# Kernel tuning notes

Hardware: AMD Instinct MI355X
Metric: run time of the kernel (lower is better)

## Reference

```python
import jax, jax.numpy as jnp
import numpy as np

B, D, H = 16384, 1024, 16
HD = D // H
EPS = 1e-5


def setup_inputs() -> dict:
    key = jax.random.key(0)
    ks = jax.random.split(key, 16)
    w = lambda k, shape: jax.random.normal(k, shape, jnp.float32) * 0.02
    return {
        "img_emb": jax.random.normal(ks[0], (B, D), jnp.float32),
        "txt_emb": jax.random.normal(ks[1], (B, D), jnp.float32),
        "route_choice": jax.random.randint(ks[2], (B,), 0, 3, jnp.int32),
        # gate: Linear(2D -> D) + sigmoid
        "Wg": w(ks[3], (2 * D, D)), "bg": jnp.zeros((D,), jnp.float32),
        # MultiheadAttention in/out projections
        "Wqkv": w(ks[4], (D, 3 * D)), "bqkv": jnp.zeros((3 * D,), jnp.float32),
        "Wo": w(ks[5], (D, D)), "bo": jnp.zeros((D,), jnp.float32),
        # LayerNorm
        "gamma": jnp.ones((D,), jnp.float32), "beta": jnp.zeros((D,), jnp.float32),
        # FFN: Linear(D->4D), GELU, Linear(4D->D)
        "Wf1": w(ks[6], (D, 4 * D)), "bf1": jnp.zeros((4 * D,), jnp.float32),
        "Wf2": w(ks[7], (4 * D, D)), "bf2": jnp.zeros((D,), jnp.float32),
    }


def _layernorm(x, gamma, beta):
    mu = jnp.mean(x, axis=-1, keepdims=True)
    var = jnp.mean(jnp.square(x - mu), axis=-1, keepdims=True)
    return (x - mu) * jax.lax.rsqrt(var + EPS) * gamma + beta


def reference(img_emb, txt_emb, route_choice, Wg, bg, Wqkv, bqkv, Wo, bo,
              gamma, beta, Wf1, bf1, Wf2, bf2):
    # Eval mode: energy_loss = 0, no dropout. Routing choice supplied as int input.
    # Compute the 'full' fusion branch densely, then select per sample.
    ri = jnp.concatenate([img_emb, txt_emb], axis=-1)          # [B, 2D]
    gate = jax.nn.sigmoid(ri @ Wg + bg)                        # [B, D]
    fused = gate * img_emb + (1.0 - gate) * txt_emb            # [B, D]

    x = jnp.stack([img_emb, txt_emb], axis=1)                  # [B, 2, D]
    qkv = x @ Wqkv + bqkv                                      # [B, 2, 3D]
    q, k, v = jnp.split(qkv, 3, axis=-1)
    q = q.reshape(B, 2, H, HD)
    k = k.reshape(B, 2, H, HD)
    v = v.reshape(B, 2, H, HD)
    scores = jnp.einsum("bqhd,bkhd->bhqk", q, k) / np.sqrt(HD) # [B, H, 2, 2]
    attn = jax.nn.softmax(scores, axis=-1)
    ctx = jnp.einsum("bhqk,bkhd->bqhd", attn, v).reshape(B, 2, D)
    attn_out = ctx @ Wo + bo                                   # [B, 2, D]

    fused = fused + attn_out.mean(axis=1)
    fused = _layernorm(fused, gamma, beta)
    full_out = jax.nn.gelu(fused @ Wf1 + bf1, approximate=False) @ Wf2 + bf2

    rc = route_choice[:, None]
    out = jnp.where(rc == 0, img_emb, jnp.where(rc == 1, txt_emb, full_out))
    return out
```

## Files before the change

kernel.cpp:

```cpp
#include <hip/hip_runtime.h>
#include <hip/hip_bf16.h>
#include <math.h>

#define NB 16384
#define DIM 1024
#define CAP 6656
#define MT 52

using bf16 = __hip_bfloat16;
typedef __attribute__((ext_vector_type(8))) short short8;
typedef __attribute__((ext_vector_type(4))) short short4v;
typedef __attribute__((ext_vector_type(4))) float float4v;

__device__ __forceinline__ void gl_lds16(const void* g, void* l) {
  __builtin_amdgcn_global_load_lds(
      (const __attribute__((address_space(1))) unsigned int*)g,
      (__attribute__((address_space(3))) unsigned int*)l, 16, 0, 0);
}

__device__ __forceinline__ short f2bf(float x) {
  __hip_bfloat16 h = __float2bfloat16(x);
  return *reinterpret_cast<short*>(&h);
}

__device__ __forceinline__ void swz(int bid, int nN, int& m0, int& n0) {
  int x = bid & 7;
  int r = bid >> 3;
  int nl = nN >> 3;
  int nLoc = r % nl;
  int m = r / nl;
  n0 = (x + 8 * nLoc) * 128;
  m0 = m * 128;
}

__global__ __launch_bounds__(256) void transpose_cast(
    const float* __restrict__ in, bf16* __restrict__ out, int K, int N) {
  __shared__ float tile[32][33];
  int n0 = blockIdx.x * 32, k0 = blockIdx.y * 32;
  int tx = threadIdx.x, ty = threadIdx.y;
#pragma unroll
  for (int i = 0; i < 32; i += 8)
    tile[ty + i][tx] = in[(size_t)(k0 + ty + i) * N + n0 + tx];
  __syncthreads();
#pragma unroll
  for (int i = 0; i < 32; i += 8)
    out[(size_t)(n0 + ty + i) * K + k0 + tx] = __float2bfloat16(tile[tx][ty + i]);
}

__global__ __launch_bounds__(256) void fill_bias(const float* __restrict__ bqkv,
                                                 const float* __restrict__ bg,
                                                 float* __restrict__ biasA,
                                                 float* __restrict__ biasB) {
  int i = blockIdx.x * 256 + threadIdx.x;
  float qv = (i < 3072) ? bqkv[i] : 0.f;
  biasA[i] = qv;
  biasB[i] = (i < 3072) ? qv : bg[i - 3072];
}

__global__ void zero_cnt(int* cnt) { if (threadIdx.x == 0) *cnt = 0; }

__global__ __launch_bounds__(256) void index_build(const int* __restrict__ route,
                                                   int* __restrict__ cnt,
                                                   int* __restrict__ idx,
                                                   int* __restrict__ pos) {
  int r = blockIdx.x * 256 + threadIdx.x;
  if (r < NB && route[r] == 2) {
    int p = atomicAdd(cnt, 1);
    idx[p] = r;
    pos[r] = p;
  }
}

__global__ __launch_bounds__(256) void gather_cast(
    const float* __restrict__ img, const float* __restrict__ txt,
    const int* __restrict__ cnt, const int* __restrict__ idx,
    bf16* __restrict__ xg, bf16* __restrict__ tg) {
  int n = blockIdx.x;
  if (n >= *cnt) return;
  int r = idx[n];
  int c = threadIdx.x * 4;
  float4 vi = *(const float4*)(img + (size_t)r * DIM + c);
  float4 vt = *(const float4*)(txt + (size_t)r * DIM + c);
  short4v pi, pt;
  pi[0] = f2bf(vi.x); pi[1] = f2bf(vi.y); pi[2] = f2bf(vi.z); pi[3] = f2bf(vi.w);
  pt[0] = f2bf(vt.x); pt[1] = f2bf(vt.y); pt[2] = f2bf(vt.z); pt[3] = f2bf(vt.w);
  *(short4v*)(xg + (size_t)n * DIM + c) = pi;
  *(short4v*)(tg + (size_t)n * DIM + c) = pt;
}

__global__ __launch_bounds__(256) void gemm_qkvg(
    const bf16* __restrict__ A0, const bf16* __restrict__ BtQ,
    const bf16* __restrict__ BtG, const float* __restrict__ bias,
    bf16* __restrict__ outp, const int* __restrict__ cntp) {
  const int cnt = *cntp;
  int m0, n0;
  swz(blockIdx.x, 32, m0, n0);
  if (m0 >= ((cnt + 127) & ~127)) return;
  alignas(16) __shared__ bf16 sA[128 * 32];
  alignas(16) __shared__ bf16 sB[128 * 32];
  const int t = threadIdx.x;
  const int wave = t >> 6, lane = t & 63;
  const int wm = (wave >> 1) * 64, wn = (wave & 1) * 64;
  const int r16 = lane & 15, quad = lane >> 4;
  const bf16* Bt = (n0 < 3072) ? BtQ + (size_t)n0 * 1024 : BtG + (size_t)(n0 - 3072) * 1024;

  float4v acc[4][4] = {};
  for (int k0 = 0; k0 < 1024; k0 += 32) {
    if (k0) __syncthreads();
#pragma unroll
    for (int j = 0; j < 2; ++j) {
      int c = t + j * 256;
      int row = c >> 2;
      int kk = k0 + (c & 3) * 8;
      gl_lds16(Bt + (size_t)row * 1024 + kk, (void*)(sB + j * 2048 + wave * 512));
      gl_lds16(A0 + (size_t)(m0 + row) * 1024 + kk, (void*)(sA + j * 2048 + wave * 512));
    }
    __syncthreads();
    short8 af[4], bfr[4];
#pragma unroll
    for (int i = 0; i < 4; ++i) {
      af[i] = *(const short8*)(sA + (wm + i * 16 + r16) * 32 + quad * 8);
      bfr[i] = *(const short8*)(sB + (wn + i * 16 + r16) * 32 + quad * 8);
    }
#pragma unroll
    for (int i = 0; i < 4; ++i)
#pragma unroll
      for (int j = 0; j < 4; ++j)
        acc[i][j] =
            __builtin_amdgcn_mfma_f32_16x16x32_bf16(af[i], bfr[j], acc[i][j], 0, 0, 0);
  }
#pragma unroll
  for (int i = 0; i < 4; ++i)
#pragma unroll
    for (int j = 0; j < 4; ++j) {
      int gcol = n0 + wn + j * 16 + r16;
      float bv = bias[gcol];
#pragma unroll
      for (int r = 0; r < 4; ++r) {
        int grow = m0 + wm + i * 16 + quad * 4 + r;
        outp[(size_t)grow * 4096 + gcol] = __float2bfloat16(acc[i][j][r] + bv);
      }
    }
}

__global__ __launch_bounds__(256) void attn_kernel(const bf16* __restrict__ qx,
                                                   const bf16* __restrict__ tx,
                                                   bf16* __restrict__ cmean,
                                                   const int* __restrict__ cntp) {
  const int cnt = *cntp;
  int gw = blockIdx.x * 4 + (threadIdx.x >> 6);
  int lane = threadIdx.x & 63;
  int n = gw >> 4, h = gw & 15;
  if (n >= ((cnt + 127) & ~127)) return;
  const bf16* b0 = qx + (size_t)n * 4096 + h * 64 + lane;
  const bf16* b1 = tx + (size_t)n * 4096 + h * 64 + lane;
  float q0 = __bfloat162float(b0[0]);
  float k0 = __bfloat162float(b0[1024]);
  float v0 = __bfloat162float(b0[2048]);
  float q1 = __bfloat162float(b1[0]);
  float k1 = __bfloat162float(b1[1024]);
  float v1 = __bfloat162float(b1[2048]);
  float s00 = q0 * k0, s01 = q0 * k1, s10 = q1 * k0, s11 = q1 * k1;
#pragma unroll
  for (int d = 32; d > 0; d >>= 1) {
    s00 += __shfl_xor(s00, d);
    s01 += __shfl_xor(s01, d);
    s10 += __shfl_xor(s10, d);
    s11 += __shfl_xor(s11, d);
  }
  const float sc = 0.125f;
  s00 *= sc; s01 *= sc; s10 *= sc; s11 *= sc;
  float m0 = fmaxf(s00, s01), m1 = fmaxf(s10, s11);
  float e00 = expf(s00 - m0), e01 = expf(s01 - m0);
  float e10 = expf(s10 - m1), e11 = expf(s11 - m1);
  float i0 = 1.f / (e00 + e01), i1 = 1.f / (e10 + e11);
  float c0 = (e00 * i0) * v0 + (e01 * i0) * v1;
  float c1 = (e10 * i1) * v0 + (e11 * i1) * v1;
  cmean[(size_t)n * DIM + h * 64 + lane] = __float2bfloat16(0.5f * (c0 + c1));
}

__global__ __launch_bounds__(256) void wo_z_kernel(
    const float* __restrict__ img, const float* __restrict__ txt,
    const bf16* __restrict__ qx, const bf16* __restrict__ tx,
    const bf16* __restrict__ WoT, const float* __restrict__ bg,
    const float* __restrict__ bo, const bf16* __restrict__ cmean,
    bf16* __restrict__ z, const int* __restrict__ cntp, const int* __restrict__ idx) {
  const int cnt = *cntp;
  int m0, n0;
  swz(blockIdx.x, 8, m0, n0);
  if (m0 >= ((cnt + 127) & ~127)) return;
  alignas(16) __shared__ bf16 sA[128 * 32];
  alignas(16) __shared__ bf16 sB[128 * 32];
  const int t = threadIdx.x;
  const int wave = t >> 6, lane = t & 63;
  const int wm = (wave >> 1) * 64, wn = (wave & 1) * 64;
  const int r16 = lane & 15, quad = lane >> 4;

  float4v acc[4][4] = {};
  for (int k0 = 0; k0 < 1024; k0 += 32) {
    if (k0) __syncthreads();
#pragma unroll
    for (int j = 0; j < 2; ++j) {
      int c = t + j * 256;
      int row = c >> 2;
      int kk = k0 + (c & 3) * 8;
      gl_lds16(WoT + (size_t)(n0 + row) * 1024 + kk, (void*)(sB + j * 2048 + wave * 512));
      gl_lds16(cmean + (size_t)(m0 + row) * 1024 + kk, (void*)(sA + j * 2048 + wave * 512));
    }
    __syncthreads();
    short8 af[4], bfr[4];
#pragma unroll
    for (int i = 0; i < 4; ++i) {
      af[i] = *(const short8*)(sA + (wm + i * 16 + r16) * 32 + quad * 8);
      bfr[i] = *(const short8*)(sB + (wn + i * 16 + r16) * 32 + quad * 8);
    }
#pragma unroll
    for (int i = 0; i < 4; ++i)
#pragma unroll
      for (int j = 0; j < 4; ++j)
        acc[i][j] =
            __builtin_amdgcn_mfma_f32_16x16x32_bf16(af[i], bfr[j], acc[i][j], 0, 0, 0);
  }
#pragma unroll
  for (int i = 0; i < 4; ++i)
#pragma unroll
    for (int j = 0; j < 4; ++j) {
      int gcol = n0 + wn + j * 16 + r16;
      float bgv = bg[gcol], bov = bo[gcol];
#pragma unroll
      for (int r = 0; r < 4; ++r) {
        int grow = m0 + wm + i * 16 + quad * 4 + r;
        float zv = 0.f;
        if (grow < cnt) {
          int orow = idx[grow];
          float gp = __bfloat162float(qx[(size_t)grow * 4096 + 3072 + gcol]) +
                     __bfloat162float(tx[(size_t)grow * 4096 + 3072 + gcol]) + bgv;
          float g = 1.f / (1.f + expf(-gp));
          size_t ii = (size_t)orow * DIM + gcol;
          float fm = g * img[ii] + (1.f - g) * txt[ii];
          zv = fm + acc[i][j][r] + bov;
        }
        z[(size_t)grow * DIM + gcol] = __float2bfloat16(zv);
      }
    }
}

__global__ __launch_bounds__(256) void ln_kernel(bf16* __restrict__ z,
                                                 const float* __restrict__ g,
                                                 const float* __restrict__ be,
                                                 const int* __restrict__ cntp) {
  const int cnt = *cntp;
  int b = blockIdx.x, t = threadIdx.x;
  if (b >= ((cnt + 127) & ~127)) return;
  bf16* zr = z + (size_t)b * DIM;
  float v[4];
  float s = 0.f, s2 = 0.f;
#pragma unroll
  for (int i = 0; i < 4; ++i) {
    float x = __bfloat162float(zr[t + 256 * i]);
    v[i] = x; s += x; s2 += x * x;
  }
#pragma unroll
  for (int d = 32; d > 0; d >>= 1) {
    s += __shfl_xor(s, d);
    s2 += __shfl_xor(s2, d);
  }
  __shared__ float rs[4], rs2[4];
  int w = t >> 6, lane = t & 63;
  if (!lane) { rs[w] = s; rs2[w] = s2; }
  __syncthreads();
  s = rs[0] + rs[1] + rs[2] + rs[3];
  s2 = rs2[0] + rs2[1] + rs2[2] + rs2[3];
  float mu = s * (1.f / 1024.f);
  float var = s2 * (1.f / 1024.f) - mu * mu;
  float r = rsqrtf(var + 1e-5f);
#pragma unroll
  for (int i = 0; i < 4; ++i) {
    int c = t + 256 * i;
    zr[c] = __float2bfloat16((v[i] - mu) * r * g[c] + be[c]);
  }
}

__global__ __launch_bounds__(256) void gemm_gelu(
    const bf16* __restrict__ A0, const bf16* __restrict__ Bt,
    const float* __restrict__ bias, bf16* __restrict__ outp,
    const int* __restrict__ cntp) {
  const int cnt = *cntp;
  int m0, n0;
  swz(blockIdx.x, 32, m0, n0);
  if (m0 >= ((cnt + 127) & ~127)) return;
  alignas(16) __shared__ bf16 sA[128 * 32];
  alignas(16) __shared__ bf16 sB[128 * 32];
  const int t = threadIdx.x;
  const int wave = t >> 6, lane = t & 63;
  const int wm = (wave >> 1) * 64, wn = (wave & 1) * 64;
  const int r16 = lane & 15, quad = lane >> 4;

  float4v acc[4][4] = {};
  for (int k0 = 0; k0 < 1024; k0 += 32) {
    if (k0) __syncthreads();
#pragma unroll
    for (int j = 0; j < 2; ++j) {
      int c = t + j * 256;
      int row = c >> 2;
      int kk = k0 + (c & 3) * 8;
      gl_lds16(Bt + (size_t)(n0 + row) * 1024 + kk, (void*)(sB + j * 2048 + wave * 512));
      gl_lds16(A0 + (size_t)(m0 + row) * 1024 + kk, (void*)(sA + j * 2048 + wave * 512));
    }
    __syncthreads();
    short8 af[4], bfr[4];
#pragma unroll
    for (int i = 0; i < 4; ++i) {
      af[i] = *(const short8*)(sA + (wm + i * 16 + r16) * 32 + quad * 8);
      bfr[i] = *(const short8*)(sB + (wn + i * 16 + r16) * 32 + quad * 8);
    }
#pragma unroll
    for (int i = 0; i < 4; ++i)
#pragma unroll
      for (int j = 0; j < 4; ++j)
        acc[i][j] =
            __builtin_amdgcn_mfma_f32_16x16x32_bf16(af[i], bfr[j], acc[i][j], 0, 0, 0);
  }
#pragma unroll
  for (int i = 0; i < 4; ++i)
#pragma unroll
    for (int j = 0; j < 4; ++j) {
      int gcol = n0 + wn + j * 16 + r16;
      float bv = bias[gcol];
#pragma unroll
      for (int r = 0; r < 4; ++r) {
        int grow = m0 + wm + i * 16 + quad * 4 + r;
        float v = acc[i][j][r] + bv;
        float gl = 0.5f * v * (1.f + erff(v * 0.70710678118654752f));
        outp[(size_t)grow * 4096 + gcol] = __float2bfloat16(gl);
      }
    }
}

__global__ __launch_bounds__(256) void gemm_splitk(
    const bf16* __restrict__ A0, const bf16* __restrict__ Bt,
    float* __restrict__ parts, const int* __restrict__ cntp) {
  const int cnt = *cntp;
  const int nblk = 8 * MT;
  int s = blockIdx.x / nblk;
  int bid = blockIdx.x % nblk;
  int m0, n0;
  swz(bid, 8, m0, n0);
  if (m0 >= ((cnt + 127) & ~127)) return;
  alignas(16) __shared__ bf16 sA[128 * 32];
  alignas(16) __shared__ bf16 sB[128 * 32];
  const int t = threadIdx.x;
  const int wave = t >> 6, lane = t & 63;
  const int wm = (wave >> 1) * 64, wn = (wave & 1) * 64;
  const int r16 = lane & 15, quad = lane >> 4;
  const int kbase = s * 2048;

  float4v acc[4][4] = {};
  for (int k0 = kbase; k0 < kbase + 2048; k0 += 32) {
    if (k0 != kbase) __syncthreads();
#pragma unroll
    for (int j = 0; j < 2; ++j) {
      int c = t + j * 256;
      int row = c >> 2;
      int kk = k0 + (c & 3) * 8;
      gl_lds16(Bt + (size_t)(n0 + row) * 4096 + kk, (void*)(sB + j * 2048 + wave * 512));
      gl_lds16(A0 + (size_t)(m0 + row) * 4096 + kk, (void*)(sA + j * 2048 + wave * 512));
    }
    __syncthreads();
    short8 af[4], bfr[4];
#pragma unroll
    for (int i = 0; i < 4; ++i) {
      af[i] = *(const short8*)(sA + (wm + i * 16 + r16) * 32 + quad * 8);
      bfr[i] = *(const short8*)(sB + (wn + i * 16 + r16) * 32 + quad * 8);
    }
#pragma unroll
    for (int i = 0; i < 4; ++i)
#pragma unroll
      for (int j = 0; j < 4; ++j)
        acc[i][j] =
            __builtin_amdgcn_mfma_f32_16x16x32_bf16(af[i], bfr[j], acc[i][j], 0, 0, 0);
  }
  float* out = parts + (size_t)s * CAP * 1024;
#pragma unroll
  for (int i = 0; i < 4; ++i)
#pragma unroll
    for (int j = 0; j < 4; ++j) {
      int gcol = n0 + wn + j * 16 + r16;
#pragma unroll
      for (int r = 0; r < 4; ++r) {
        int grow = m0 + wm + i * 16 + quad * 4 + r;
        out[(size_t)grow * 1024 + gcol] = acc[i][j][r];
      }
    }
}

__global__ __launch_bounds__(256) void route_out(
    const float* __restrict__ img, const float* __restrict__ txt,
    const int* __restrict__ route, const int* __restrict__ pos,
    const float* __restrict__ parts, const float* __restrict__ bf2,
    float* __restrict__ out) {
  int row = blockIdx.x;
  int rc = route[row];
  int c = threadIdx.x * 4;
  float4 v;
  if (rc == 2) {
    int n = pos[row];
    float4 p0 = *(const float4*)(parts + (size_t)n * 1024 + c);
    float4 p1 = *(const float4*)(parts + (size_t)CAP * 1024 + (size_t)n * 1024 + c);
    float4 b = *(const float4*)(bf2 + c);
    v.x = p0.x + p1.x + b.x;
    v.y = p0.y + p1.y + b.y;
    v.z = p0.z + p1.z + b.z;
    v.w = p0.w + p1.w + b.w;
  } else {
    const float* src = (rc == 0) ? img : txt;
    v = *(const float4*)(src + (size_t)row * DIM + c);
  }
  *(float4*)(out + (size_t)row * DIM + c) = v;
}

extern "C" void kernel_launch(void* const* d_in, const int* in_sizes, int n_in,
                              void* d_out, int out_size, void* d_ws, size_t ws_size,
                              hipStream_t stream) {
  const float* img = (const float*)d_in[0];
  const float* txt = (const float*)d_in[1];
  const int* route = (const int*)d_in[2];
  const float* Wg = (const float*)d_in[3];
  const float* bg = (const float*)d_in[4];
  const float* Wqkv = (const float*)d_in[5];
  const float* bqkv = (const float*)d_in[6];
  const float* Wo = (const float*)d_in[7];
  const float* bo = (const float*)d_in[8];
  const float* gamma = (const float*)d_in[9];
  const float* beta = (const float*)d_in[10];
  const float* Wf1 = (const float*)d_in[11];
  const float* bf1 = (const float*)d_in[12];
  const float* Wf2 = (const float*)d_in[13];
  const float* bf2 = (const float*)d_in[14];

  char* ws = (char*)d_ws;
  size_t off = 0;
  auto alloc = [&](size_t bytes) {
    char* p = ws + off;
    off += (bytes + 255) & ~(size_t)255;
    return p;
  };
  int* cntp = (int*)alloc(256);
  int* idx = (int*)alloc((size_t)NB * 4);
  int* pos = (int*)alloc((size_t)NB * 4);
  float* biasA = (float*)alloc(4096 * 4);
  float* biasB = (float*)alloc(4096 * 4);
  bf16* WqkvT = (bf16*)alloc((size_t)3072 * 1024 * 2);
  bf16* WgTopT = (bf16*)alloc((size_t)1024 * 1024 * 2);
  bf16* WgBotT = (bf16*)alloc((size_t)1024 * 1024 * 2);
  bf16* WoT = (bf16*)alloc((size_t)1024 * 1024 * 2);
  bf16* Wf1T = (bf16*)alloc((size_t)4096 * 1024 * 2);
  bf16* Wf2T = (bf16*)alloc((size_t)1024 * 4096 * 2);
  bf16* xg = (bf16*)alloc((size_t)CAP * 1024 * 2);
  bf16* tg = (bf16*)alloc((size_t)CAP * 1024 * 2);
  bf16* qx = (bf16*)alloc((size_t)CAP * 4096 * 2);
  bf16* tx = (bf16*)alloc((size_t)CAP * 4096 * 2);
  bf16* cmean = (bf16*)alloc((size_t)CAP * 1024 * 2);
  bf16* zb = (bf16*)alloc((size_t)CAP * 1024 * 2);
  bf16* hb = qx;
  float* parts = (float*)tx;

  dim3 tblk(32, 8);
  transpose_cast<<<dim3(3072 / 32, 1024 / 32), tblk, 0, stream>>>(Wqkv, WqkvT, 1024, 3072);
  transpose_cast<<<dim3(1024 / 32, 1024 / 32), tblk, 0, stream>>>(Wg, WgTopT, 1024, 1024);
  transpose_cast<<<dim3(1024 / 32, 1024 / 32), tblk, 0, stream>>>(Wg + 1024 * 1024, WgBotT, 1024, 1024);
  transpose_cast<<<dim3(1024 / 32, 1024 / 32), tblk, 0, stream>>>(Wo, WoT, 1024, 1024);
  transpose_cast<<<dim3(4096 / 32, 1024 / 32), tblk, 0, stream>>>(Wf1, Wf1T, 1024, 4096);
  transpose_cast<<<dim3(1024 / 32, 4096 / 32), tblk, 0, stream>>>(Wf2, Wf2T, 4096, 1024);
  fill_bias<<<16, 256, 0, stream>>>(bqkv, bg, biasA, biasB);

  zero_cnt<<<1, 64, 0, stream>>>(cntp);
  index_build<<<NB / 256, 256, 0, stream>>>(route, cntp, idx, pos);
  gather_cast<<<CAP, 256, 0, stream>>>(img, txt, cntp, idx, xg, tg);

  gemm_qkvg<<<32 * MT, 256, 0, stream>>>(xg, WqkvT, WgTopT, biasA, qx, cntp);
  gemm_qkvg<<<32 * MT, 256, 0, stream>>>(tg, WqkvT, WgBotT, biasB, tx, cntp);
  attn_kernel<<<CAP * 4, 256, 0, stream>>>(qx, tx, cmean, cntp);
  wo_z_kernel<<<8 * MT, 256, 0, stream>>>(img, txt, qx, tx, WoT, bg, bo, cmean, zb,
                                          cntp, idx);
  ln_kernel<<<CAP, 256, 0, stream>>>(zb, gamma, beta, cntp);
  gemm_gelu<<<32 * MT, 256, 0, stream>>>(zb, Wf1T, bf1, hb, cntp);
  gemm_splitk<<<2 * 8 * MT, 256, 0, stream>>>(hb, Wf2T, parts, cntp);
  route_out<<<NB, 256, 0, stream>>>(img, txt, route, pos, parts, bf2, (float*)d_out);
}
```

Baseline: 595.7 us.

## Fuse prep kernels, swizzle LDS tiles, merge QKV GEMMs, atomic split-K output

Merges the six weight transpose-casts, the bias fill and the counter reset into one prep kernel to cut launch count. Applies an XOR swizzle to the LDS tile layout in every GEMM, so fragment reads avoid bank conflicts. Merges the two QKV/gate GEMMs into a single 2D-grid launch. Replaces the split-K partial buffer and the route_out combine with a pre-fill of the output (passthrough rows or bias) plus atomicAdd scatter from the split-K GEMM, which adds atomic traffic and makes the summation order nondeterministic.

```diff
diff --git a/kernel.cpp b/kernel.cpp
--- a/kernel.cpp
+++ b/kernel.cpp
@@ -33,41 +33,64 @@
   m0 = m * 128;
 }
 
-__global__ __launch_bounds__(256) void transpose_cast(
-    const float* __restrict__ in, bf16* __restrict__ out, int K, int N) {
-  __shared__ float tile[32][33];
-  int n0 = blockIdx.x * 32, k0 = blockIdx.y * 32;
+#define STAGE_TILE(SRC, LD, DST)                                              \
+  {                                                                           \
+    int row = c >> 2, sslot = c & 3;                                          \
+    int kp = sslot ^ (row & 3);                                               \
+    gl_lds16((SRC) + (size_t)row * (LD) + k0 + kp * 8,                        \
+             (void*)((DST) + j * 2048 + wave * 512));                         \
+  }
+
+__device__ __forceinline__ void tr_tile(const float* in, bf16* out, int K, int N,
+                                        int tile) {
+  __shared__ float tl[32][33];
+  int nx = N / 32;
+  int n0 = (tile % nx) * 32, k0 = (tile / nx) * 32;
   int tx = threadIdx.x, ty = threadIdx.y;
 #pragma unroll
   for (int i = 0; i < 32; i += 8)
-    tile[ty + i][tx] = in[(size_t)(k0 + ty + i) * N + n0 + tx];
+    tl[ty + i][tx] = in[(size_t)(k0 + ty + i) * N + n0 + tx];
   __syncthreads();
 #pragma unroll
   for (int i = 0; i < 32; i += 8)
-    out[(size_t)(n0 + ty + i) * K + k0 + tx] = __float2bfloat16(tile[tx][ty + i]);
-}
-
-__global__ __launch_bounds__(256) void fill_bias(const float* __restrict__ bqkv,
-                                                 const float* __restrict__ bg,
-                                                 float* __restrict__ biasA,
-                                                 float* __restrict__ biasB) {
-  int i = blockIdx.x * 256 + threadIdx.x;
+    out[(size_t)(n0 + ty + i) * K + k0 + tx] = __float2bfloat16(tl[tx][ty + i]);
+}
+
+__global__ __launch_bounds__(256) void prep_kernel(
+    const float* __restrict__ Wqkv, const float* __restrict__ Wg,
+    const float* __restrict__ Wo, const float* __restrict__ Wf1,
+    const float* __restrict__ Wf2, const float* __restrict__ bqkv,
+    const float* __restrict__ bg, bf16* __restrict__ WqkvT,
+    bf16* __restrict__ WgTopT, bf16* __restrict__ WgBotT, bf16* __restrict__ WoT,
+    bf16* __restrict__ Wf1T, bf16* __restrict__ Wf2T, float* __restrict__ biasA,
+    float* __restrict__ biasB, int* __restrict__ cnt) {
+  int bid = blockIdx.x;
+  if (bid == 0 && threadIdx.x == 0 && threadIdx.y == 0) *cnt = 0;
+  if (bid < 3072) { tr_tile(Wqkv, WqkvT, 1024, 3072, bid); return; }
+  bid -= 3072;
+  if (bid < 1024) { tr_tile(Wg, WgTopT, 1024, 1024, bid); return; }
+  bid -= 1024;
+  if (bid < 1024) { tr_tile(Wg + 1024 * 1024, WgBotT, 1024, 1024, bid); return; }
+  bid -= 1024;
+  if (bid < 1024) { tr_tile(Wo, WoT, 1024, 1024, bid); return; }
+  bid -= 1024;
+  if (bid < 4096) { tr_tile(Wf1, Wf1T, 1024, 4096, bid); return; }
+  bid -= 4096;
+  if (bid < 4096) { tr_tile(Wf2, Wf2T, 4096, 1024, bid); return; }
+  bid -= 4096;
+  int i = bid * 256 + threadIdx.y * 32 + threadIdx.x;
   float qv = (i < 3072) ? bqkv[i] : 0.f;
   biasA[i] = qv;
   biasB[i] = (i < 3072) ? qv : bg[i - 3072];
 }
 
-__global__ void zero_cnt(int* cnt) { if (threadIdx.x == 0) *cnt = 0; }
-
 __global__ __launch_bounds__(256) void index_build(const int* __restrict__ route,
                                                    int* __restrict__ cnt,
-                                                   int* __restrict__ idx,
-                                                   int* __restrict__ pos) {
+                                                   int* __restrict__ idx) {
   int r = blockIdx.x * 256 + threadIdx.x;
   if (r < NB && route[r] == 2) {
     int p = atomicAdd(cnt, 1);
     idx[p] = r;
-    pos[r] = p;
   }
 }
 
@@ -89,19 +112,27 @@
 }
 
 __global__ __launch_bounds__(256) void gemm_qkvg(
-    const bf16* __restrict__ A0, const bf16* __restrict__ BtQ,
-    const bf16* __restrict__ BtG, const float* __restrict__ bias,
-    bf16* __restrict__ outp, const int* __restrict__ cntp) {
+    const bf16* __restrict__ xg, const bf16* __restrict__ tg,
+    const bf16* __restrict__ BtQ, const bf16* __restrict__ BtGT,
+    const bf16* __restrict__ BtGB, const float* __restrict__ biasA,
+    const float* __restrict__ biasB, bf16* __restrict__ qx,
+    bf16* __restrict__ tx, const int* __restrict__ cntp) {
   const int cnt = *cntp;
   int m0, n0;
   swz(blockIdx.x, 32, m0, n0);
   if (m0 >= ((cnt + 127) & ~127)) return;
+  const int src = blockIdx.y;
+  const bf16* A0 = src ? tg : xg;
+  const bf16* BtG = src ? BtGB : BtGT;
+  const float* bias = src ? biasB : biasA;
+  bf16* outp = src ? tx : qx;
   alignas(16) __shared__ bf16 sA[128 * 32];
   alignas(16) __shared__ bf16 sB[128 * 32];
   const int t = threadIdx.x;
   const int wave = t >> 6, lane = t & 63;
   const int wm = (wave >> 1) * 64, wn = (wave & 1) * 64;
   const int r16 = lane & 15, quad = lane >> 4;
+  const int sl = (quad ^ (r16 & 3)) * 8;
   const bf16* Bt = (n0 < 3072) ? BtQ + (size_t)n0 * 1024 : BtG + (size_t)(n0 - 3072) * 1024;
 
   float4v acc[4][4] = {};
@@ -110,17 +141,15 @@
 #pragma unroll
     for (int j = 0; j < 2; ++j) {
       int c = t + j * 256;
-      int row = c >> 2;
-      int kk = k0 + (c & 3) * 8;
-      gl_lds16(Bt + (size_t)row * 1024 + kk, (void*)(sB + j * 2048 + wave * 512));
-      gl_lds16(A0 + (size_t)(m0 + row) * 1024 + kk, (void*)(sA + j * 2048 + wave * 512));
+      STAGE_TILE(Bt, 1024, sB)
+      STAGE_TILE(A0 + (size_t)m0 * 1024, 1024, sA)
     }
     __syncthreads();
     short8 af[4], bfr[4];
 #pragma unroll
     for (int i = 0; i < 4; ++i) {
-      af[i] = *(const short8*)(sA + (wm + i * 16 + r16) * 32 + quad * 8);
-      bfr[i] = *(const short8*)(sB + (wn + i * 16 + r16) * 32 + quad * 8);
+      af[i] = *(const short8*)(sA + (wm + i * 16 + r16) * 32 + sl);
+      bfr[i] = *(const short8*)(sB + (wn + i * 16 + r16) * 32 + sl);
     }
 #pragma unroll
     for (int i = 0; i < 4; ++i)
@@ -137,7 +166,7 @@
       float bv = bias[gcol];
 #pragma unroll
       for (int r = 0; r < 4; ++r) {
-        int grow = m0 + wm + i * 16 + quad * 4 + r;
+        int grow = m0 + wm + i * 16 + (lane >> 4) * 4 + r;
         outp[(size_t)grow * 4096 + gcol] = __float2bfloat16(acc[i][j][r] + bv);
       }
     }
@@ -195,6 +224,7 @@
   const int wave = t >> 6, lane = t & 63;
   const int wm = (wave >> 1) * 64, wn = (wave & 1) * 64;
   const int r16 = lane & 15, quad = lane >> 4;
+  const int sl = (quad ^ (r16 & 3)) * 8;
 
   float4v acc[4][4] = {};
   for (int k0 = 0; k0 < 1024; k0 += 32) {
@@ -202,17 +232,15 @@
 #pragma unroll
     for (int j = 0; j < 2; ++j) {
       int c = t + j * 256;
-      int row = c >> 2;
-      int kk = k0 + (c & 3) * 8;
-      gl_lds16(WoT + (size_t)(n0 + row) * 1024 + kk, (void*)(sB + j * 2048 + wave * 512));
-      gl_lds16(cmean + (size_t)(m0 + row) * 1024 + kk, (void*)(sA + j * 2048 + wave * 512));
+      STAGE_TILE(WoT + (size_t)n0 * 1024, 1024, sB)
+      STAGE_TILE(cmean + (size_t)m0 * 1024, 1024, sA)
     }
     __syncthreads();
     short8 af[4], bfr[4];
 #pragma unroll
     for (int i = 0; i < 4; ++i) {
-      af[i] = *(const short8*)(sA + (wm + i * 16 + r16) * 32 + quad * 8);
-      bfr[i] = *(const short8*)(sB + (wn + i * 16 + r16) * 32 + quad * 8);
+      af[i] = *(const short8*)(sA + (wm + i * 16 + r16) * 32 + sl);
+      bfr[i] = *(const short8*)(sB + (wn + i * 16 + r16) * 32 + sl);
     }
 #pragma unroll
     for (int i = 0; i < 4; ++i)
@@ -295,6 +323,7 @@
   const int wave = t >> 6, lane = t & 63;
   const int wm = (wave >> 1) * 64, wn = (wave & 1) * 64;
   const int r16 = lane & 15, quad = lane >> 4;
+  const int sl = (quad ^ (r16 & 3)) * 8;
 
   float4v acc[4][4] = {};
   for (int k0 = 0; k0 < 1024; k0 += 32) {
@@ -302,17 +331,15 @@
 #pragma unroll
     for (int j = 0; j < 2; ++j) {
       int c = t + j * 256;
-      int row = c >> 2;
-      int kk = k0 + (c & 3) * 8;
-      gl_lds16(Bt + (size_t)(n0 + row) * 1024 + kk, (void*)(sB + j * 2048 + wave * 512));
-      gl_lds16(A0 + (size_t)(m0 + row) * 1024 + kk, (void*)(sA + j * 2048 + wave * 512));
+      STAGE_TILE(Bt + (size_t)n0 * 1024, 1024, sB)
+      STAGE_TILE(A0 + (size_t)m0 * 1024, 1024, sA)
     }
     __syncthreads();
     short8 af[4], bfr[4];
 #pragma unroll
     for (int i = 0; i < 4; ++i) {
-      af[i] = *(const short8*)(sA + (wm + i * 16 + r16) * 32 + quad * 8);
-      bfr[i] = *(const short8*)(sB + (wn + i * 16 + r16) * 32 + quad * 8);
+      af[i] = *(const short8*)(sA + (wm + i * 16 + r16) * 32 + sl);
+      bfr[i] = *(const short8*)(sB + (wn + i * 16 + r16) * 32 + sl);
     }
 #pragma unroll
     for (int i = 0; i < 4; ++i)
@@ -337,23 +364,39 @@
     }
 }
 
+__global__ __launch_bounds__(256) void route_pre(
+    const float* __restrict__ img, const float* __restrict__ txt,
+    const int* __restrict__ route, const float* __restrict__ bf2,
+    float* __restrict__ out) {
+  int row = blockIdx.x;
+  int rc = route[row];
+  int c = threadIdx.x * 4;
+  float4 v;
+  if (rc == 2) {
+    v = *(const float4*)(bf2 + c);
+  } else {
+    const float* src = (rc == 0) ? img : txt;
+    v = *(const float4*)(src + (size_t)row * DIM + c);
+  }
+  *(float4*)(out + (size_t)row * DIM + c) = v;
+}
+
 __global__ __launch_bounds__(256) void gemm_splitk(
     const bf16* __restrict__ A0, const bf16* __restrict__ Bt,
-    float* __restrict__ parts, const int* __restrict__ cntp) {
-  const int cnt = *cntp;
-  const int nblk = 8 * MT;
-  int s = blockIdx.x / nblk;
-  int bid = blockIdx.x % nblk;
+    float* __restrict__ out, const int* __restrict__ cntp,
+    const int* __restrict__ idx) {
+  const int cnt = *cntp;
   int m0, n0;
-  swz(bid, 8, m0, n0);
+  swz(blockIdx.x, 8, m0, n0);
   if (m0 >= ((cnt + 127) & ~127)) return;
+  const int kbase = blockIdx.y * 2048;
   alignas(16) __shared__ bf16 sA[128 * 32];
   alignas(16) __shared__ bf16 sB[128 * 32];
   const int t = threadIdx.x;
   const int wave = t >> 6, lane = t & 63;
   const int wm = (wave >> 1) * 64, wn = (wave & 1) * 64;
   const int r16 = lane & 15, quad = lane >> 4;
-  const int kbase = s * 2048;
+  const int sl = (quad ^ (r16 & 3)) * 8;
 
   float4v acc[4][4] = {};
   for (int k0 = kbase; k0 < kbase + 2048; k0 += 32) {
@@ -361,17 +404,15 @@
 #pragma unroll
     for (int j = 0; j < 2; ++j) {
       int c = t + j * 256;
-      int row = c >> 2;
-      int kk = k0 + (c & 3) * 8;
-      gl_lds16(Bt + (size_t)(n0 + row) * 4096 + kk, (void*)(sB + j * 2048 + wave * 512));
-      gl_lds16(A0 + (size_t)(m0 + row) * 4096 + kk, (void*)(sA + j * 2048 + wave * 512));
+      STAGE_TILE(Bt + (size_t)n0 * 4096, 4096, sB)
+      STAGE_TILE(A0 + (size_t)m0 * 4096, 4096, sA)
     }
     __syncthreads();
     short8 af[4], bfr[4];
 #pragma unroll
     for (int i = 0; i < 4; ++i) {
-      af[i] = *(const short8*)(sA + (wm + i * 16 + r16) * 32 + quad * 8);
-      bfr[i] = *(const short8*)(sB + (wn + i * 16 + r16) * 32 + quad * 8);
+      af[i] = *(const short8*)(sA + (wm + i * 16 + r16) * 32 + sl);
+      bfr[i] = *(const short8*)(sB + (wn + i * 16 + r16) * 32 + sl);
     }
 #pragma unroll
     for (int i = 0; i < 4; ++i)
@@ -380,7 +421,6 @@
         acc[i][j] =
             __builtin_amdgcn_mfma_f32_16x16x32_bf16(af[i], bfr[j], acc[i][j], 0, 0, 0);
   }
-  float* out = parts + (size_t)s * CAP * 1024;
 #pragma unroll
   for (int i = 0; i < 4; ++i)
 #pragma unroll
@@ -389,34 +429,12 @@
 #pragma unroll
       for (int r = 0; r < 4; ++r) {
         int grow = m0 + wm + i * 16 + quad * 4 + r;
-        out[(size_t)grow * 1024 + gcol] = acc[i][j][r];
+        if (grow < cnt) {
+          int orow = idx[grow];
+          atomicAdd(out + (size_t)orow * DIM + gcol, acc[i][j][r]);
+        }
       }
     }
-}
-
-__global__ __launch_bounds__(256) void route_out(
-    const float* __restrict__ img, const float* __restrict__ txt,
-    const int* __restrict__ route, const int* __restrict__ pos,
-    const float* __restrict__ parts, const float* __restrict__ bf2,
-    float* __restrict__ out) {
-  int row = blockIdx.x;
-  int rc = route[row];
-  int c = threadIdx.x * 4;
-  float4 v;
-  if (rc == 2) {
-    int n = pos[row];
-    float4 p0 = *(const float4*)(parts + (size_t)n * 1024 + c);
-    float4 p1 = *(const float4*)(parts + (size_t)CAP * 1024 + (size_t)n * 1024 + c);
-    float4 b = *(const float4*)(bf2 + c);
-    v.x = p0.x + p1.x + b.x;
-    v.y = p0.y + p1.y + b.y;
-    v.z = p0.z + p1.z + b.z;
-    v.w = p0.w + p1.w + b.w;
-  } else {
-    const float* src = (rc == 0) ? img : txt;
-    v = *(const float4*)(src + (size_t)row * DIM + c);
-  }
-  *(float4*)(out + (size_t)row * DIM + c) = v;
 }
 
 extern "C" void kernel_launch(void* const* d_in, const int* in_sizes, int n_in,
@@ -447,7 +465,6 @@
   };
   int* cntp = (int*)alloc(256);
   int* idx = (int*)alloc((size_t)NB * 4);
-  int* pos = (int*)alloc((size_t)NB * 4);
   float* biasA = (float*)alloc(4096 * 4);
   float* biasB = (float*)alloc(4096 * 4);
   bf16* WqkvT = (bf16*)alloc((size_t)3072 * 1024 * 2);
@@ -463,28 +480,20 @@
   bf16* cmean = (bf16*)alloc((size_t)CAP * 1024 * 2);
   bf16* zb = (bf16*)alloc((size_t)CAP * 1024 * 2);
   bf16* hb = qx;
-  float* parts = (float*)tx;
-
-  dim3 tblk(32, 8);
-  transpose_cast<<<dim3(3072 / 32, 1024 / 32), tblk, 0, stream>>>(Wqkv, WqkvT, 1024, 3072);
-  transpose_cast<<<dim3(1024 / 32, 1024 / 32), tblk, 0, stream>>>(Wg, WgTopT, 1024, 1024);
-  transpose_cast<<<dim3(1024 / 32, 1024 / 32), tblk, 0, stream>>>(Wg + 1024 * 1024, WgBotT, 1024, 1024);
-  transpose_cast<<<dim3(1024 / 32, 1024 / 32), tblk, 0, stream>>>(Wo, WoT, 1024, 1024);
-  transpose_cast<<<dim3(4096 / 32, 1024 / 32), tblk, 0, stream>>>(Wf1, Wf1T, 1024, 4096);
-  transpose_cast<<<dim3(1024 / 32, 4096 / 32), tblk, 0, stream>>>(Wf2, Wf2T, 4096, 1024);
-  fill_bias<<<16, 256, 0, stream>>>(bqkv, bg, biasA, biasB);
-
-  zero_cnt<<<1, 64, 0, stream>>>(cntp);
-  index_build<<<NB / 256, 256, 0, stream>>>(route, cntp, idx, pos);
+
+  prep_kernel<<<14352, dim3(32, 8), 0, stream>>>(
+      Wqkv, Wg, Wo, Wf1, Wf2, bqkv, bg, WqkvT, WgTopT, WgBotT, WoT, Wf1T, Wf2T,
+      biasA, biasB, cntp);
+  index_build<<<NB / 256, 256, 0, stream>>>(route, cntp, idx);
   gather_cast<<<CAP, 256, 0, stream>>>(img, txt, cntp, idx, xg, tg);
 
-  gemm_qkvg<<<32 * MT, 256, 0, stream>>>(xg, WqkvT, WgTopT, biasA, qx, cntp);
-  gemm_qkvg<<<32 * MT, 256, 0, stream>>>(tg, WqkvT, WgBotT, biasB, tx, cntp);
+  gemm_qkvg<<<dim3(32 * MT, 2), 256, 0, stream>>>(xg, tg, WqkvT, WgTopT, WgBotT,
+                                                  biasA, biasB, qx, tx, cntp);
   attn_kernel<<<CAP * 4, 256, 0, stream>>>(qx, tx, cmean, cntp);
   wo_z_kernel<<<8 * MT, 256, 0, stream>>>(img, txt, qx, tx, WoT, bg, bo, cmean, zb,
                                           cntp, idx);
   ln_kernel<<<CAP, 256, 0, stream>>>(zb, gamma, beta, cntp);
   gemm_gelu<<<32 * MT, 256, 0, stream>>>(zb, Wf1T, bf1, hb, cntp);
-  gemm_splitk<<<2 * 8 * MT, 256, 0, stream>>>(hb, Wf2T, parts, cntp);
-  route_out<<<NB, 256, 0, stream>>>(img, txt, route, pos, parts, bf2, (float*)d_out);
-}
+  route_pre<<<NB, 256, 0, stream>>>(img, txt, route, bf2, (float*)d_out);
+  gemm_splitk<<<dim3(8 * MT, 2), 256, 0, stream>>>(hb, Wf2T, (float*)d_out, cntp, idx);
+}
```

Result: slower. 619.9 us (+4.1%).
